# Performance work log

Measured on AMD Instinct MI355X. Metric: run time of the kernel, lower is better.

## Reference

```python
import jax, jax.numpy as jnp
import numpy as np

B, D, N, K = 4, 256, 4096, 8192


def setup_inputs() -> dict:
    key = jax.random.key(0)
    kx, ke = jax.random.split(key)
    x = jax.random.normal(kx, (B, D, N), dtype=jnp.float32)
    e = jax.random.normal(ke, (K, D), dtype=jnp.float32)
    return {"x": x, "e": e}


def reference(x, e):
    # encode: cdist(x^T [B,N,D], e [K,D]) -> [B,N,K]; argmin over K.
    # sqrt is monotonic, so argmin of squared distance == argmin of cdist.
    xt = jnp.transpose(x, (0, 2, 1))                      # [B,N,D]
    x2 = jnp.sum(xt * xt, axis=-1, keepdims=True)         # [B,N,1]
    e2 = jnp.sum(e * e, axis=-1)                          # [K]
    d2 = x2 - 2.0 * jnp.einsum('bnd,kd->bnk', xt, e) + e2 # [B,N,K]
    codes = jnp.argmin(d2, axis=-1)                       # [B,N]
    # decode: embedding gather then transpose back to [B,D,N]
    quantized = e[codes]                                  # [B,N,D]
    return jnp.transpose(quantized, (0, 2, 1))            # [B,D,N]
```

## Files before the change

### kernel.cpp

```cpp
#include <hip/hip_runtime.h>
#include <stdint.h>

#define B_ 4
#define D_ 256
#define N_ 4096
#define K_ 8192
#define Q_ (B_*N_)

#define KSPLIT_ 4
#define KSLICE_ (K_/KSPLIT_)
#define NCHUNK_ (KSLICE_/32)
#define QTILE_ 128

typedef __attribute__((ext_vector_type(8))) short bf16x8;
typedef __attribute__((ext_vector_type(16))) float f32x16;

__device__ __forceinline__ unsigned short f32_to_bf16(float f) {
  unsigned u = __float_as_uint(f);
  unsigned r = 0x7FFFu + ((u >> 16) & 1u);
  return (unsigned short)((u + r) >> 16);
}
__device__ __forceinline__ float bf16_to_f32(unsigned short h) {
  return __uint_as_float(((unsigned)h) << 16);
}

__device__ __forceinline__ void gl_lds16(const void* g, void* l) {
  __builtin_amdgcn_global_load_lds(
      (const __attribute__((address_space(1))) unsigned int*)g,
      (__attribute__((address_space(3))) unsigned int*)l, 16, 0, 0);
}

__global__ void prep_x_kernel(const float* __restrict__ x,
                              unsigned short* __restrict__ xh,
                              unsigned short* __restrict__ xl) {
  __shared__ float tile[32][33];
  int b = blockIdx.z;
  int d0 = blockIdx.y * 32;
  int n0 = blockIdx.x * 32;
  int tx = threadIdx.x, ty = threadIdx.y;
  const float* xp = x + ((size_t)b * D_ + d0) * N_ + n0;
#pragma unroll
  for (int i = 0; i < 4; ++i)
    tile[ty + 8 * i][tx] = xp[(size_t)(ty + 8 * i) * N_ + tx];
  __syncthreads();
#pragma unroll
  for (int i = 0; i < 4; ++i) {
    int nl = ty + 8 * i;
    float v = tile[tx][nl];
    unsigned short h = f32_to_bf16(v);
    unsigned short l = f32_to_bf16(v - bf16_to_f32(h));
    size_t q = (size_t)b * N_ + n0 + nl;
    xh[q * D_ + d0 + tx] = h;
    xl[q * D_ + d0 + tx] = l;
  }
}

__global__ void prep_e_kernel(const float* __restrict__ e,
                              unsigned short* __restrict__ eh,
                              unsigned short* __restrict__ el,
                              float* __restrict__ e2h,
                              unsigned long long* __restrict__ keys) {
  int k = blockIdx.x;
  int d = threadIdx.x;
  if (d < 2) keys[(size_t)k * 2 + d] = ~0ull;
  float v = e[(size_t)k * D_ + d];
  unsigned short h = f32_to_bf16(v);
  unsigned short l = f32_to_bf16(v - bf16_to_f32(h));
  eh[(size_t)k * D_ + d] = h;
  el[(size_t)k * D_ + d] = l;
  float s = v * v;
#pragma unroll
  for (int off = 32; off > 0; off >>= 1) s += __shfl_down(s, off, 64);
  __shared__ float ws4[4];
  if ((threadIdx.x & 63) == 0) ws4[threadIdx.x >> 6] = s;
  __syncthreads();
  if (threadIdx.x == 0) e2h[k] = 0.5f * (ws4[0] + ws4[1] + ws4[2] + ws4[3]);
}

__global__ __launch_bounds__(256, 2) void vq_main_kernel(
    const unsigned short* __restrict__ xh, const unsigned short* __restrict__ xl,
    const unsigned short* __restrict__ eh, const unsigned short* __restrict__ el,
    const float* __restrict__ e2h, unsigned long long* __restrict__ keys) {
  __shared__ __attribute__((aligned(16))) unsigned short Bs[2][2][32 * 256];

  const int tid = threadIdx.x;
  const int w = tid >> 6;
  const int lane = tid & 63;
  const int l = lane & 31;
  const int hi = lane >> 5;

  const int qt = blockIdx.x >> 2;
  const int ksl = blockIdx.x & 3;
  const int q0 = qt * QTILE_;
  const int kbase = ksl * KSLICE_;
  const int qw = q0 + w * 32;

  bf16x8 ah[16], al[16];
  {
    const unsigned short* pa = xh + (size_t)(qw + l) * D_ + hi * 8;
    const unsigned short* pb = xl + (size_t)(qw + l) * D_ + hi * 8;
#pragma unroll
    for (int kc16 = 0; kc16 < 16; ++kc16) {
      ah[kc16] = *(const bf16x8*)(pa + kc16 * 16);
      al[kc16] = *(const bf16x8*)(pb + kc16 * 16);
    }
  }

  float rminv[16];
  int rmini[16];
#pragma unroll
  for (int r = 0; r < 16; ++r) { rminv[r] = __builtin_inff(); rmini[r] = 0; }

  auto stage = [&](int ch, int buf) {
    const int kc = kbase + ch * 32;
#pragma unroll
    for (int p = 0; p < 4; ++p) {
      const int c0 = w * 8 + p * 2;
      const int c = c0 + hi;
      const int g = l ^ (c & 31);
      const size_t srcoff = (size_t)(kc + c) * D_ + g * 8;
      gl_lds16(eh + srcoff, &Bs[buf][0][c0 * 256]);
      gl_lds16(el + srcoff, &Bs[buf][1][c0 * 256]);
    }
  };

  stage(0, 0);

#pragma unroll 1
  for (int ch = 0; ch < NCHUNK_; ++ch) {
    const int buf = ch & 1;
    __syncthreads();
    if (ch + 1 < NCHUNK_) stage(ch + 1, buf ^ 1);
    const int kc = kbase + ch * 32;
    const float e2v = e2h[kc + l];

    f32x16 acc;
#pragma unroll
    for (int r = 0; r < 16; ++r) acc[r] = 0.f;

#pragma unroll
    for (int ks = 0; ks < 16; ++ks) {
      const int pos = (((ks * 2 + hi) ^ l) * 8);
      bf16x8 bh = *(const bf16x8*)&Bs[buf][0][l * 256 + pos];
      bf16x8 bl = *(const bf16x8*)&Bs[buf][1][l * 256 + pos];
      acc = __builtin_amdgcn_mfma_f32_32x32x16_bf16(ah[ks], bh, acc, 0, 0, 0);
      acc = __builtin_amdgcn_mfma_f32_32x32x16_bf16(ah[ks], bl, acc, 0, 0, 0);
      acc = __builtin_amdgcn_mfma_f32_32x32x16_bf16(al[ks], bh, acc, 0, 0, 0);
    }

    const int kidx = kc + l;
#pragma unroll
    for (int r = 0; r < 16; ++r) {
      float dv = e2v - acc[r];
      bool better = dv < rminv[r];
      rminv[r] = better ? dv : rminv[r];
      rmini[r] = better ? kidx : rmini[r];
    }
  }

#pragma unroll
  for (int r = 0; r < 16; ++r) {
    float bv = rminv[r];
    int bi = rmini[r];
#pragma unroll
    for (int xm = 1; xm <= 16; xm <<= 1) {
      float ov = __shfl_xor(bv, xm, 64);
      int oi = __shfl_xor(bi, xm, 64);
      if (ov < bv || (ov == bv && oi < bi)) { bv = ov; bi = oi; }
    }
    if (l == 0) {
      const int m = (r & 3) + 8 * (r >> 2) + 4 * hi;
      const int qq = qw + m;
      unsigned su = __float_as_uint(bv);
      su ^= (unsigned)(((int)su >> 31) | 0x80000000u);
      unsigned long long key = ((unsigned long long)su << 32) | (unsigned)bi;
      atomicMin(keys + qq, key);
    }
  }
}

__global__ void decode_kernel(const unsigned long long* __restrict__ keys,
                              const float* __restrict__ e,
                              float* __restrict__ out) {
  __shared__ float tile[32][33];
  __shared__ int codes[32];
  int b = blockIdx.y;
  int n0 = blockIdx.x * 32;
  int tx = threadIdx.x, ty = threadIdx.y;
  if (ty == 0)
    codes[tx] = (int)(keys[(size_t)b * N_ + n0 + tx] & 0xFFFFFFFFull);
  __syncthreads();
#pragma unroll 1
  for (int d0 = 0; d0 < D_; d0 += 32) {
#pragma unroll
    for (int i = 0; i < 4; ++i) {
      int nl = ty + 8 * i;
      tile[nl][tx] = e[(size_t)codes[nl] * D_ + d0 + tx];
    }
    __syncthreads();
#pragma unroll
    for (int i = 0; i < 4; ++i) {
      int dl = ty + 8 * i;
      out[((size_t)b * D_ + d0 + dl) * N_ + n0 + tx] = tile[tx][dl];
    }
    __syncthreads();
  }
}

extern "C" void kernel_launch(void* const* d_in, const int* in_sizes, int n_in,
                              void* d_out, int out_size, void* d_ws, size_t ws_size,
                              hipStream_t stream) {
  const float* x = (const float*)d_in[0];
  const float* e = (const float*)d_in[1];
  float* out = (float*)d_out;

  char* wksp = (char*)d_ws;
  unsigned short* xh = (unsigned short*)wksp;
  unsigned short* xl = xh + (size_t)Q_ * D_;
  unsigned short* eh = xl + (size_t)Q_ * D_;
  unsigned short* el = eh + (size_t)K_ * D_;
  float* e2h = (float*)(el + (size_t)K_ * D_);
  unsigned long long* keys = (unsigned long long*)(e2h + K_);

  prep_x_kernel<<<dim3(N_ / 32, D_ / 32, B_), dim3(32, 8), 0, stream>>>(x, xh, xl);
  prep_e_kernel<<<K_, 256, 0, stream>>>(e, eh, el, e2h, keys);
  vq_main_kernel<<<512, 256, 0, stream>>>(xh, xl, eh, el, e2h, keys);
  decode_kernel<<<dim3(N_ / 32, B_), dim3(32, 8), 0, stream>>>(keys, e, out);
}
```

Before: 264.3 us.

## Process two 32-row query tiles per wave to reuse codebook fragments

Each wave now holds A fragments for 64 queries and runs two independent MFMA accumulator chains against the same LDS-loaded codebook fragments, doubling the query tile per block to 256. This halves LDS reads per MFMA and exposes instruction-level parallelism between the two chains. In exchange, register usage roughly doubles and launch bounds drop to one block per CU, which lowers occupancy and risks register spilling.

```diff
diff --git a/kernel.cpp b/kernel.cpp
--- a/kernel.cpp
+++ b/kernel.cpp
@@ -10,7 +10,7 @@
 #define KSPLIT_ 4
 #define KSLICE_ (K_/KSPLIT_)
 #define NCHUNK_ (KSLICE_/32)
-#define QTILE_ 128
+#define QTILE_ 256
 
 typedef __attribute__((ext_vector_type(8))) short bf16x8;
 typedef __attribute__((ext_vector_type(16))) float f32x16;
@@ -77,7 +77,7 @@
   if (threadIdx.x == 0) e2h[k] = 0.5f * (ws4[0] + ws4[1] + ws4[2] + ws4[3]);
 }
 
-__global__ __launch_bounds__(256, 2) void vq_main_kernel(
+__global__ __launch_bounds__(256, 1) void vq_main_kernel(
     const unsigned short* __restrict__ xh, const unsigned short* __restrict__ xl,
     const unsigned short* __restrict__ eh, const unsigned short* __restrict__ el,
     const float* __restrict__ e2h, unsigned long long* __restrict__ keys) {
@@ -93,23 +93,30 @@
   const int ksl = blockIdx.x & 3;
   const int q0 = qt * QTILE_;
   const int kbase = ksl * KSLICE_;
-  const int qw = q0 + w * 32;
-
-  bf16x8 ah[16], al[16];
+  const int qw = q0 + w * 64;
+
+  bf16x8 ah0[16], al0[16], ah1[16], al1[16];
   {
-    const unsigned short* pa = xh + (size_t)(qw + l) * D_ + hi * 8;
-    const unsigned short* pb = xl + (size_t)(qw + l) * D_ + hi * 8;
+    const unsigned short* p0h = xh + (size_t)(qw + l) * D_ + hi * 8;
+    const unsigned short* p0l = xl + (size_t)(qw + l) * D_ + hi * 8;
+    const unsigned short* p1h = xh + (size_t)(qw + 32 + l) * D_ + hi * 8;
+    const unsigned short* p1l = xl + (size_t)(qw + 32 + l) * D_ + hi * 8;
 #pragma unroll
     for (int kc16 = 0; kc16 < 16; ++kc16) {
-      ah[kc16] = *(const bf16x8*)(pa + kc16 * 16);
-      al[kc16] = *(const bf16x8*)(pb + kc16 * 16);
-    }
-  }
-
-  float rminv[16];
-  int rmini[16];
-#pragma unroll
-  for (int r = 0; r < 16; ++r) { rminv[r] = __builtin_inff(); rmini[r] = 0; }
+      ah0[kc16] = *(const bf16x8*)(p0h + kc16 * 16);
+      al0[kc16] = *(const bf16x8*)(p0l + kc16 * 16);
+      ah1[kc16] = *(const bf16x8*)(p1h + kc16 * 16);
+      al1[kc16] = *(const bf16x8*)(p1l + kc16 * 16);
+    }
+  }
+
+  float rminv0[16], rminv1[16];
+  int rmini0[16], rmini1[16];
+#pragma unroll
+  for (int r = 0; r < 16; ++r) {
+    rminv0[r] = __builtin_inff(); rmini0[r] = 0;
+    rminv1[r] = __builtin_inff(); rmini1[r] = 0;
+  }
 
   auto stage = [&](int ch, int buf) {
     const int kc = kbase + ch * 32;
@@ -134,47 +141,71 @@
     const int kc = kbase + ch * 32;
     const float e2v = e2h[kc + l];
 
-    f32x16 acc;
-#pragma unroll
-    for (int r = 0; r < 16; ++r) acc[r] = 0.f;
+    f32x16 acc0, acc1;
+#pragma unroll
+    for (int r = 0; r < 16; ++r) { acc0[r] = 0.f; acc1[r] = 0.f; }
 
 #pragma unroll
     for (int ks = 0; ks < 16; ++ks) {
       const int pos = (((ks * 2 + hi) ^ l) * 8);
       bf16x8 bh = *(const bf16x8*)&Bs[buf][0][l * 256 + pos];
       bf16x8 bl = *(const bf16x8*)&Bs[buf][1][l * 256 + pos];
-      acc = __builtin_amdgcn_mfma_f32_32x32x16_bf16(ah[ks], bh, acc, 0, 0, 0);
-      acc = __builtin_amdgcn_mfma_f32_32x32x16_bf16(ah[ks], bl, acc, 0, 0, 0);
-      acc = __builtin_amdgcn_mfma_f32_32x32x16_bf16(al[ks], bh, acc, 0, 0, 0);
+      acc0 = __builtin_amdgcn_mfma_f32_32x32x16_bf16(ah0[ks], bh, acc0, 0, 0, 0);
+      acc1 = __builtin_amdgcn_mfma_f32_32x32x16_bf16(ah1[ks], bh, acc1, 0, 0, 0);
+      acc0 = __builtin_amdgcn_mfma_f32_32x32x16_bf16(ah0[ks], bl, acc0, 0, 0, 0);
+      acc1 = __builtin_amdgcn_mfma_f32_32x32x16_bf16(ah1[ks], bl, acc1, 0, 0, 0);
+      acc0 = __builtin_amdgcn_mfma_f32_32x32x16_bf16(al0[ks], bh, acc0, 0, 0, 0);
+      acc1 = __builtin_amdgcn_mfma_f32_32x32x16_bf16(al1[ks], bh, acc1, 0, 0, 0);
     }
 
     const int kidx = kc + l;
 #pragma unroll
     for (int r = 0; r < 16; ++r) {
-      float dv = e2v - acc[r];
-      bool better = dv < rminv[r];
-      rminv[r] = better ? dv : rminv[r];
-      rmini[r] = better ? kidx : rmini[r];
+      float dv0 = e2v - acc0[r];
+      bool b0 = dv0 < rminv0[r];
+      rminv0[r] = b0 ? dv0 : rminv0[r];
+      rmini0[r] = b0 ? kidx : rmini0[r];
+      float dv1 = e2v - acc1[r];
+      bool b1 = dv1 < rminv1[r];
+      rminv1[r] = b1 ? dv1 : rminv1[r];
+      rmini1[r] = b1 ? kidx : rmini1[r];
     }
   }
 
 #pragma unroll
   for (int r = 0; r < 16; ++r) {
-    float bv = rminv[r];
-    int bi = rmini[r];
-#pragma unroll
-    for (int xm = 1; xm <= 16; xm <<= 1) {
-      float ov = __shfl_xor(bv, xm, 64);
-      int oi = __shfl_xor(bi, xm, 64);
-      if (ov < bv || (ov == bv && oi < bi)) { bv = ov; bi = oi; }
-    }
-    if (l == 0) {
-      const int m = (r & 3) + 8 * (r >> 2) + 4 * hi;
-      const int qq = qw + m;
-      unsigned su = __float_as_uint(bv);
-      su ^= (unsigned)(((int)su >> 31) | 0x80000000u);
-      unsigned long long key = ((unsigned long long)su << 32) | (unsigned)bi;
-      atomicMin(keys + qq, key);
+    const int m = (r & 3) + 8 * (r >> 2) + 4 * hi;
+    {
+      float bv = rminv0[r];
+      int bi = rmini0[r];
+#pragma unroll
+      for (int xm = 1; xm <= 16; xm <<= 1) {
+        float ov = __shfl_xor(bv, xm, 64);
+        int oi = __shfl_xor(bi, xm, 64);
+        if (ov < bv || (ov == bv && oi < bi)) { bv = ov; bi = oi; }
+      }
+      if (l == 0) {
+        unsigned su = __float_as_uint(bv);
+        su ^= (unsigned)(((int)su >> 31) | 0x80000000u);
+        unsigned long long key = ((unsigned long long)su << 32) | (unsigned)bi;
+        atomicMin(keys + (qw + m), key);
+      }
+    }
+    {
+      float bv = rminv1[r];
+      int bi = rmini1[r];
+#pragma unroll
+      for (int xm = 1; xm <= 16; xm <<= 1) {
+        float ov = __shfl_xor(bv, xm, 64);
+        int oi = __shfl_xor(bi, xm, 64);
+        if (ov < bv || (ov == bv && oi < bi)) { bv = ov; bi = oi; }
+      }
+      if (l == 0) {
+        unsigned su = __float_as_uint(bv);
+        su ^= (unsigned)(((int)su >> 31) | 0x80000000u);
+        unsigned long long key = ((unsigned long long)su << 32) | (unsigned)bi;
+        atomicMin(keys + (qw + 32 + m), key);
+      }
     }
   }
 }
@@ -224,6 +255,6 @@
 
   prep_x_kernel<<<dim3(N_ / 32, D_ / 32, B_), dim3(32, 8), 0, stream>>>(x, xh, xl);
   prep_e_kernel<<<K_, 256, 0, stream>>>(e, eh, el, e2h, keys);
-  vq_main_kernel<<<512, 256, 0, stream>>>(xh, xl, eh, el, e2h, keys);
+  vq_main_kernel<<<(Q_ / QTILE_) * KSPLIT_, 256, 0, stream>>>(xh, xl, eh, el, e2h, keys);
   decode_kernel<<<dim3(N_ / 32, B_), dim3(32, 8), 0, stream>>>(keys, e, out);
 }
```

Result: slower. 271.3 us (+2.6%).

## Enlarge VQ tiles to 256 queries by 64 codes and fold e2 into accumulator init

Applied to the files above, without the earlier changes.

Doubles the query tile to 256 rows with 512 threads (8 waves) and the codebook chunk to 64 codes, so each staged LDS chunk feeds twice as many MFMAs. x is negated during prep so the accumulator can start at e2/2 and the subtraction after the MMA goes away. This cuts codebook reloads per query and per-element epilogue work, but doubles LDS use to 128KB per block, which may limit occupancy. The stage lambda still loads only 32 rows per pass with 8 waves covering 64, so its indexing needs to match the new layout.

```diff
diff --git a/kernel.cpp b/kernel.cpp
--- a/kernel.cpp
+++ b/kernel.cpp
@@ -9,8 +9,9 @@
 
 #define KSPLIT_ 4
 #define KSLICE_ (K_/KSPLIT_)
-#define NCHUNK_ (KSLICE_/32)
-#define QTILE_ 128
+#define CHUNK_ 64
+#define NCHUNK_ (KSLICE_/CHUNK_)
+#define QTILE_ 256
 
 typedef __attribute__((ext_vector_type(8))) short bf16x8;
 typedef __attribute__((ext_vector_type(16))) float f32x16;
@@ -46,7 +47,7 @@
 #pragma unroll
   for (int i = 0; i < 4; ++i) {
     int nl = ty + 8 * i;
-    float v = tile[tx][nl];
+    float v = -tile[tx][nl];
     unsigned short h = f32_to_bf16(v);
     unsigned short l = f32_to_bf16(v - bf16_to_f32(h));
     size_t q = (size_t)b * N_ + n0 + nl;
@@ -77,11 +78,11 @@
   if (threadIdx.x == 0) e2h[k] = 0.5f * (ws4[0] + ws4[1] + ws4[2] + ws4[3]);
 }
 
-__global__ __launch_bounds__(256, 2) void vq_main_kernel(
+__global__ __launch_bounds__(512, 2) void vq_main_kernel(
     const unsigned short* __restrict__ xh, const unsigned short* __restrict__ xl,
     const unsigned short* __restrict__ eh, const unsigned short* __restrict__ el,
     const float* __restrict__ e2h, unsigned long long* __restrict__ keys) {
-  __shared__ __attribute__((aligned(16))) unsigned short Bs[2][2][32 * 256];
+  __shared__ __attribute__((aligned(16))) unsigned short Bs[2][2][CHUNK_ * 256];
 
   const int tid = threadIdx.x;
   const int w = tid >> 6;
@@ -112,7 +113,7 @@
   for (int r = 0; r < 16; ++r) { rminv[r] = __builtin_inff(); rmini[r] = 0; }
 
   auto stage = [&](int ch, int buf) {
-    const int kc = kbase + ch * 32;
+    const int kc = kbase + ch * CHUNK_;
 #pragma unroll
     for (int p = 0; p < 4; ++p) {
       const int c0 = w * 8 + p * 2;
@@ -131,30 +132,52 @@
     const int buf = ch & 1;
     __syncthreads();
     if (ch + 1 < NCHUNK_) stage(ch + 1, buf ^ 1);
-    const int kc = kbase + ch * 32;
-    const float e2v = e2h[kc + l];
-
-    f32x16 acc;
-#pragma unroll
-    for (int r = 0; r < 16; ++r) acc[r] = 0.f;
-
-#pragma unroll
-    for (int ks = 0; ks < 16; ++ks) {
-      const int pos = (((ks * 2 + hi) ^ l) * 8);
-      bf16x8 bh = *(const bf16x8*)&Bs[buf][0][l * 256 + pos];
-      bf16x8 bl = *(const bf16x8*)&Bs[buf][1][l * 256 + pos];
-      acc = __builtin_amdgcn_mfma_f32_32x32x16_bf16(ah[ks], bh, acc, 0, 0, 0);
-      acc = __builtin_amdgcn_mfma_f32_32x32x16_bf16(ah[ks], bl, acc, 0, 0, 0);
-      acc = __builtin_amdgcn_mfma_f32_32x32x16_bf16(al[ks], bh, acc, 0, 0, 0);
-    }
-
-    const int kidx = kc + l;
-#pragma unroll
-    for (int r = 0; r < 16; ++r) {
-      float dv = e2v - acc[r];
-      bool better = dv < rminv[r];
-      rminv[r] = better ? dv : rminv[r];
-      rmini[r] = better ? kidx : rmini[r];
+    const int kc = kbase + ch * CHUNK_;
+    const float e2v0 = e2h[kc + l];
+    const float e2v1 = e2h[kc + 32 + l];
+
+    {
+      f32x16 acc;
+#pragma unroll
+      for (int r = 0; r < 16; ++r) acc[r] = e2v0;
+#pragma unroll
+      for (int ks = 0; ks < 16; ++ks) {
+        const int pos = (((ks * 2 + hi) ^ l) * 8);
+        bf16x8 bh = *(const bf16x8*)&Bs[buf][0][l * 256 + pos];
+        bf16x8 bl = *(const bf16x8*)&Bs[buf][1][l * 256 + pos];
+        acc = __builtin_amdgcn_mfma_f32_32x32x16_bf16(ah[ks], bh, acc, 0, 0, 0);
+        acc = __builtin_amdgcn_mfma_f32_32x32x16_bf16(ah[ks], bl, acc, 0, 0, 0);
+        acc = __builtin_amdgcn_mfma_f32_32x32x16_bf16(al[ks], bh, acc, 0, 0, 0);
+      }
+      const int kidx = kc + l;
+#pragma unroll
+      for (int r = 0; r < 16; ++r) {
+        bool better = acc[r] < rminv[r];
+        rminv[r] = better ? acc[r] : rminv[r];
+        rmini[r] = better ? kidx : rmini[r];
+      }
+    }
+
+    {
+      f32x16 acc;
+#pragma unroll
+      for (int r = 0; r < 16; ++r) acc[r] = e2v1;
+#pragma unroll
+      for (int ks = 0; ks < 16; ++ks) {
+        const int pos = (((ks * 2 + hi) ^ l) * 8);
+        bf16x8 bh = *(const bf16x8*)&Bs[buf][0][(32 + l) * 256 + pos];
+        bf16x8 bl = *(const bf16x8*)&Bs[buf][1][(32 + l) * 256 + pos];
+        acc = __builtin_amdgcn_mfma_f32_32x32x16_bf16(ah[ks], bh, acc, 0, 0, 0);
+        acc = __builtin_amdgcn_mfma_f32_32x32x16_bf16(ah[ks], bl, acc, 0, 0, 0);
+        acc = __builtin_amdgcn_mfma_f32_32x32x16_bf16(al[ks], bh, acc, 0, 0, 0);
+      }
+      const int kidx = kc + 32 + l;
+#pragma unroll
+      for (int r = 0; r < 16; ++r) {
+        bool better = acc[r] < rminv[r];
+        rminv[r] = better ? acc[r] : rminv[r];
+        rmini[r] = better ? kidx : rmini[r];
+      }
     }
   }
 
@@ -224,6 +247,6 @@
 
   prep_x_kernel<<<dim3(N_ / 32, D_ / 32, B_), dim3(32, 8), 0, stream>>>(x, xh, xl);
   prep_e_kernel<<<K_, 256, 0, stream>>>(e, eh, el, e2h, keys);
-  vq_main_kernel<<<512, 256, 0, stream>>>(xh, xl, eh, el, e2h, keys);
+  vq_main_kernel<<<(Q_ / QTILE_) * KSPLIT_, 512, 0, stream>>>(xh, xl, eh, el, e2h, keys);
   decode_kernel<<<dim3(N_ / 32, B_), dim3(32, 8), 0, stream>>>(keys, e, out);
 }
```

New measurement: 252.8 us. 1.05x faster.
